# Optimization experiments

Hardware: AMD Instinct MI355X
Metric: run time of the kernel (lower is better)

## Reference

```python
import jax, jax.numpy as jnp
import numpy as np

TABLE_SZ = 2 ** 14
FEAT_DIM = 2
NUM_LEVELS = 16
MIN_RES = 16.0
MAX_RES = 512.0
B = 1 << 20

# corner order v0..v7 from get_nearest_vertices_coords (z-ascending, ccw)
OFFSETS = jnp.array([[0, 0, 0], [1, 0, 0], [1, 1, 0], [0, 1, 0],
                     [0, 0, 1], [1, 0, 1], [1, 1, 1], [0, 1, 1]], dtype=jnp.int32)


def setup_inputs() -> dict:
    key = jax.random.key(0)
    kx, kt = jax.random.split(key)
    x = jax.random.uniform(kx, (B, 3), dtype=jnp.float32)  # coords in [0,1)
    # RandomUniform(-1e-4, 1e-4) initializer for all 16 tables, stacked
    tables = jax.random.uniform(kt, (NUM_LEVELS, TABLE_SZ, FEAT_DIM),
                                dtype=jnp.float32, minval=-1e-4, maxval=1e-4)
    return {"x": x, "tables": tables}


def reference(x, tables):
    # per-level resolutions: floor(min_res * b**l), b geometric growth factor
    b = jnp.exp((jnp.log(MAX_RES) - jnp.log(MIN_RES)) / (NUM_LEVELS - 1))
    res = jnp.floor(MIN_RES * b ** jnp.arange(NUM_LEVELS, dtype=jnp.float32))  # [L]

    # NOTE: original computes interp weights from the UNSCALED position
    # (position - floor(position)); since x in [0,1) this equals x. Faithful.
    w = x - jnp.floor(x)  # [B,3]
    off = OFFSETS.astype(bool)[None]  # [1,8,3]
    # trilinear weight per corner: prod over xyz of (w if offset else 1-w)
    cw = jnp.prod(jnp.where(off, w[:, None, :], 1.0 - w[:, None, :]), axis=-1)  # [B,8]

    P1 = jnp.uint32(2654435761)
    P2 = jnp.uint32(805459861)
    TS = jnp.uint32(TABLE_SZ)

    def level(carry, lvl):
        table, r = lvl  # [T,F], scalar
        sp = r * x  # [B,3]
        low = jnp.floor(sp).astype(jnp.int32)
        high = jnp.ceil(sp).astype(jnp.int32)
        corners = jnp.where(off, high[:, None, :], low[:, None, :]).astype(jnp.uint32)  # [B,8,3]
        # spatial hash: x ^ (p1*y) ^ (p2*z) mod table_sz (uint32 wraparound;
        # table_sz is a power of two so this matches int32-wrap + floormod)
        h = (corners[..., 0] ^ (P1 * corners[..., 1]) ^ (P2 * corners[..., 2])) % TS
        feats = table[h.astype(jnp.int32)]  # gather -> [B,8,F]
        return carry, jnp.einsum('bkf,bk->bf', feats, cw)  # [B,F]

    _, outs = jax.lax.scan(level, None, (tables, res))  # [L,B,F]
    # matches tf.concat over levels along feature axis
    return jnp.transpose(outs, (1, 0, 2)).reshape(x.shape[0], NUM_LEVELS * FEAT_DIM)
```

## Files before the change

kernel.cpp:

```cpp
#include <hip/hip_runtime.h>
#include <cmath>

#define TABLE_SZ 16384
#define NLEV 16
#define BLOCK 256
#define PPT 4
#define HALF 8

struct ResArr { float r[NLEV]; };

__global__ __launch_bounds__(256) void cvt_tables(
    const float* __restrict__ src, uint32_t* __restrict__ dst, int n_entries)
{
    int i = blockIdx.x * blockDim.x + threadIdx.x;
    int e = i * 4;
    if (e + 3 < n_entries) {
        const float4* s4 = (const float4*)(src) + i * 2;
        float4 a = s4[0], b = s4[1];
        uint32_t o[4];
        float v[8] = {a.x,a.y,a.z,a.w,b.x,b.y,b.z,b.w};
        #pragma unroll
        for (int k = 0; k < 4; ++k) {
            uint32_t lo = __float_as_uint(v[2*k+0]);
            uint32_t hi = __float_as_uint(v[2*k+1]);
            lo = (lo + 0x7FFFu + ((lo >> 16) & 1u)) >> 16;
            hi = (hi + 0x7FFFu + ((hi >> 16) & 1u)) & 0xFFFF0000u;
            o[k] = lo | hi;
        }
        *(uint4*)(dst + e) = make_uint4(o[0], o[1], o[2], o[3]);
    }
}

template <typename T>
__device__ __forceinline__ void stage_level(const T* __restrict__ gsrc,
                                            size_t level_bytes, int l,
                                            void* lds, int tid, int wid)
{
    const char* gbase = (const char*)gsrc + (size_t)l * level_bytes;
    const int rounds = (int)(level_bytes / (BLOCK * 16));
    #pragma unroll
    for (int j = 0; j < 16; ++j) {
        if (j >= rounds) break;
        uint32_t goff = (uint32_t)(j * (BLOCK * 16) + tid * 16);
        uint32_t loff = (uint32_t)(j * (BLOCK * 16) + wid * 1024);
        __builtin_amdgcn_global_load_lds(
            (const __attribute__((address_space(1))) uint32_t*)(gbase + goff),
            (__attribute__((address_space(3))) uint32_t*)((char*)lds + loff),
            16, 0, 0);
    }
}

__device__ __forceinline__ float2 level_accum_bf(const uint32_t* tab, float r,
                                                 float px, float py, float pz)
{
    const uint32_t P1 = 2654435761u, P2 = 805459861u;
    const uint32_t m  = TABLE_SZ - 1u;

    float ax = 1.0f - px, ay = 1.0f - py, az = 1.0f - pz;
    float sx = r*px, sy = r*py, sz = r*pz;
    uint32_t lx = (uint32_t)(int32_t)floorf(sx);
    uint32_t hx = (uint32_t)(int32_t)ceilf(sx);
    uint32_t ly = (uint32_t)(int32_t)floorf(sy);
    uint32_t hy = (uint32_t)(int32_t)ceilf(sy);
    uint32_t lz = (uint32_t)(int32_t)floorf(sz);
    uint32_t hz = (uint32_t)(int32_t)ceilf(sz);
    uint32_t yl = P1*ly, yh = P1*hy;
    uint32_t zl = P2*lz, zh = P2*hz;

    float a0, a1;
    {
        uint32_t v0 = tab[(lx ^ yl ^ zl) & m];
        uint32_t v1 = tab[(hx ^ yl ^ zl) & m];
        uint32_t v2 = tab[(hx ^ yh ^ zl) & m];
        uint32_t v3 = tab[(lx ^ yh ^ zl) & m];
        float cw0 = (ax*ay)*az;
        float cw1 = (px*ay)*az;
        float cw2 = (px*py)*az;
        float cw3 = (ax*py)*az;
        a0  = __uint_as_float(v0 << 16)        * cw0;
        a1  = __uint_as_float(v0 & 0xFFFF0000u) * cw0;
        a0 += __uint_as_float(v1 << 16)        * cw1;
        a1 += __uint_as_float(v1 & 0xFFFF0000u) * cw1;
        a0 += __uint_as_float(v2 << 16)        * cw2;
        a1 += __uint_as_float(v2 & 0xFFFF0000u) * cw2;
        a0 += __uint_as_float(v3 << 16)        * cw3;
        a1 += __uint_as_float(v3 & 0xFFFF0000u) * cw3;
    }
    {
        uint32_t v4 = tab[(lx ^ yl ^ zh) & m];
        uint32_t v5 = tab[(hx ^ yl ^ zh) & m];
        uint32_t v6 = tab[(hx ^ yh ^ zh) & m];
        uint32_t v7 = tab[(lx ^ yh ^ zh) & m];
        float cw4 = (ax*ay)*pz;
        float cw5 = (px*ay)*pz;
        float cw6 = (px*py)*pz;
        float cw7 = (ax*py)*pz;
        a0 += __uint_as_float(v4 << 16)        * cw4;
        a1 += __uint_as_float(v4 & 0xFFFF0000u) * cw4;
        a0 += __uint_as_float(v5 << 16)        * cw5;
        a1 += __uint_as_float(v5 & 0xFFFF0000u) * cw5;
        a0 += __uint_as_float(v6 << 16)        * cw6;
        a1 += __uint_as_float(v6 & 0xFFFF0000u) * cw6;
        a0 += __uint_as_float(v7 << 16)        * cw7;
        a1 += __uint_as_float(v7 & 0xFFFF0000u) * cw7;
    }
    return make_float2(a0, a1);
}

__device__ __forceinline__ float2 level_accum_f32(const float2* tab, float r,
                                                  float px, float py, float pz)
{
    const uint32_t P1 = 2654435761u, P2 = 805459861u;
    const uint32_t m  = TABLE_SZ - 1u;
    float ax = 1.0f - px, ay = 1.0f - py, az = 1.0f - pz;
    float sx = r*px, sy = r*py, sz = r*pz;
    uint32_t lx = (uint32_t)(int32_t)floorf(sx);
    uint32_t hx = (uint32_t)(int32_t)ceilf(sx);
    uint32_t ly = (uint32_t)(int32_t)floorf(sy);
    uint32_t hy = (uint32_t)(int32_t)ceilf(sy);
    uint32_t lz = (uint32_t)(int32_t)floorf(sz);
    uint32_t hz = (uint32_t)(int32_t)ceilf(sz);
    uint32_t yl = P1*ly, yh = P1*hy;
    uint32_t zl = P2*lz, zh = P2*hz;
    float a0, a1;
    {
        float2 f0 = tab[(lx ^ yl ^ zl) & m];
        float2 f1 = tab[(hx ^ yl ^ zl) & m];
        float2 f2 = tab[(hx ^ yh ^ zl) & m];
        float2 f3 = tab[(lx ^ yh ^ zl) & m];
        float cw0 = (ax*ay)*az, cw1 = (px*ay)*az, cw2 = (px*py)*az, cw3 = (ax*py)*az;
        a0  = f0.x*cw0;  a1  = f0.y*cw0;
        a0 += f1.x*cw1;  a1 += f1.y*cw1;
        a0 += f2.x*cw2;  a1 += f2.y*cw2;
        a0 += f3.x*cw3;  a1 += f3.y*cw3;
    }
    {
        float2 f4 = tab[(lx ^ yl ^ zh) & m];
        float2 f5 = tab[(hx ^ yl ^ zh) & m];
        float2 f6 = tab[(hx ^ yh ^ zh) & m];
        float2 f7 = tab[(lx ^ yh ^ zh) & m];
        float cw4 = (ax*ay)*pz, cw5 = (px*ay)*pz, cw6 = (px*py)*pz, cw7 = (ax*py)*pz;
        a0 += f4.x*cw4;  a1 += f4.y*cw4;
        a0 += f5.x*cw5;  a1 += f5.y*cw5;
        a0 += f6.x*cw6;  a1 += f6.y*cw6;
        a0 += f7.x*cw7;  a1 += f7.y*cw7;
    }
    return make_float2(a0, a1);
}

__global__ __launch_bounds__(BLOCK) void mrhe_bf(
    const float* __restrict__ x,
    const uint32_t* __restrict__ tb,
    float* __restrict__ out,
    ResArr res, int B)
{
    __shared__ uint32_t tab[TABLE_SZ];

    const int tid  = threadIdx.x;
    const int wid  = tid >> 6;
    const int base = blockIdx.x * (BLOCK * PPT);

    float px[PPT], py[PPT], pz[PPT];
    #pragma unroll
    for (int p = 0; p < PPT; ++p) {
        int idx = base + p * BLOCK + tid;
        size_t j = (idx < B) ? (size_t)idx : 0;
        px[p] = x[3*j+0]; py[p] = x[3*j+1]; pz[p] = x[3*j+2];
    }

    #pragma unroll
    for (int half = 0; half < NLEV / HALF; ++half) {
        float o[PPT][2*HALF];

        #pragma unroll
        for (int hl = 0; hl < HALF; ++hl) {
            const int l = half * HALF + hl;
            __syncthreads();
            stage_level(tb, (size_t)TABLE_SZ * 4, l, tab, tid, wid);
            __syncthreads();

            const float r = res.r[l];
            #pragma unroll
            for (int p = 0; p < PPT; ++p) {
                float2 a = level_accum_bf(tab, r, px[p], py[p], pz[p]);
                o[p][2*hl+0] = a.x;
                o[p][2*hl+1] = a.y;
            }
        }

        #pragma unroll
        for (int p = 0; p < PPT; ++p) {
            int idx = base + p * BLOCK + tid;
            if (idx < B) {
                float* po = out + (size_t)idx * (2*NLEV) + half * (2*HALF);
                #pragma unroll
                for (int j = 0; j < (2*HALF)/4; ++j) {
                    float4 v;
                    v.x = o[p][4*j+0]; v.y = o[p][4*j+1];
                    v.z = o[p][4*j+2]; v.w = o[p][4*j+3];
                    ((float4*)po)[j] = v;
                }
            }
        }
    }
}

#define PPTF 2
__global__ __launch_bounds__(BLOCK) void mrhe_f32(
    const float* __restrict__ x,
    const float* __restrict__ tables,
    float* __restrict__ out,
    ResArr res, int B)
{
    __shared__ float2 tab[TABLE_SZ];

    const int tid  = threadIdx.x;
    const int wid  = tid >> 6;
    const int base = blockIdx.x * (BLOCK * PPTF);

    float px[PPTF], py[PPTF], pz[PPTF];
    #pragma unroll
    for (int p = 0; p < PPTF; ++p) {
        int idx = base + p * BLOCK + tid;
        size_t j = (idx < B) ? (size_t)idx : 0;
        px[p] = x[3*j+0]; py[p] = x[3*j+1]; pz[p] = x[3*j+2];
    }

    #pragma unroll
    for (int half = 0; half < NLEV / HALF; ++half) {
        float o[PPTF][2*HALF];
        #pragma unroll
        for (int hl = 0; hl < HALF; ++hl) {
            const int l = half * HALF + hl;
            __syncthreads();
            {
                const char* gbase = (const char*)tables + (size_t)l * (TABLE_SZ * 8);
                #pragma unroll
                for (int j = 0; j < (TABLE_SZ * 8) / (BLOCK * 16); ++j) {
                    uint32_t goff = (uint32_t)(j * (BLOCK * 16) + tid * 16);
                    uint32_t loff = (uint32_t)(j * (BLOCK * 16) + wid * 1024);
                    __builtin_amdgcn_global_load_lds(
                        (const __attribute__((address_space(1))) uint32_t*)(gbase + goff),
                        (__attribute__((address_space(3))) uint32_t*)((char*)tab + loff),
                        16, 0, 0);
                }
            }
            __syncthreads();
            const float r = res.r[l];
            #pragma unroll
            for (int p = 0; p < PPTF; ++p) {
                float2 a = level_accum_f32(tab, r, px[p], py[p], pz[p]);
                o[p][2*hl+0] = a.x;
                o[p][2*hl+1] = a.y;
            }
        }
        #pragma unroll
        for (int p = 0; p < PPTF; ++p) {
            int idx = base + p * BLOCK + tid;
            if (idx < B) {
                float* po = out + (size_t)idx * (2*NLEV) + half * (2*HALF);
                #pragma unroll
                for (int j = 0; j < (2*HALF)/4; ++j) {
                    float4 v;
                    v.x = o[p][4*j+0]; v.y = o[p][4*j+1];
                    v.z = o[p][4*j+2]; v.w = o[p][4*j+3];
                    ((float4*)po)[j] = v;
                }
            }
        }
    }
}

extern "C" void kernel_launch(void* const* d_in, const int* in_sizes, int n_in,
                              void* d_out, int out_size, void* d_ws, size_t ws_size,
                              hipStream_t stream)
{
    const float* x      = (const float*)d_in[0];
    const float* tables = (const float*)d_in[1];
    float* out = (float*)d_out;
    int B = in_sizes[0] / 3;

    ResArr res;
    float bgrow = expf((logf(512.0f) - logf(16.0f)) / 15.0f);
    for (int l = 0; l < NLEV; ++l)
        res.r[l] = floorf(16.0f * powf(bgrow, (float)l));

    const int n_entries = NLEV * TABLE_SZ;
    const size_t need = (size_t)n_entries * 4;

    if (ws_size >= need && d_ws) {
        uint32_t* tb = (uint32_t*)d_ws;
        hipLaunchKernelGGL(cvt_tables, dim3(n_entries/4/256), dim3(256), 0, stream,
                           tables, tb, n_entries);
        int per_block = BLOCK * PPT;
        int grid = (B + per_block - 1) / per_block;
        hipLaunchKernelGGL(mrhe_bf, dim3(grid), dim3(BLOCK), 0, stream,
                           x, tb, out, res, B);
    } else {
        int per_block = BLOCK * PPTF;
        int grid = (B + per_block - 1) / per_block;
        hipLaunchKernelGGL(mrhe_f32, dim3(grid), dim3(BLOCK), 0, stream,
                           x, tables, out, res, B);
    }
}
```

Before: 133.8 us.

## Double-buffer per-level hash table staging in LDS to overlap loads with gathers

Replaces the single LDS table buffer with two buffers. The next level's table is prefetched with global_load_lds while the current level is interpolated, using manual vmcnt waits and raw s_barrier in place of the two __syncthreads per level. The aim is to hide the table staging latency behind the gather and accumulate work. The cost is that LDS use per block doubles to 128KB, which likely limits the CU to a single 256-thread block and leaves fewer waves to hide LDS gather latency.

```diff
diff --git a/kernel.cpp b/kernel.cpp
--- a/kernel.cpp
+++ b/kernel.cpp
@@ -31,21 +31,17 @@
     }
 }
 
-template <typename T>
-__device__ __forceinline__ void stage_level(const T* __restrict__ gsrc,
-                                            size_t level_bytes, int l,
-                                            void* lds, int tid, int wid)
-{
-    const char* gbase = (const char*)gsrc + (size_t)l * level_bytes;
-    const int rounds = (int)(level_bytes / (BLOCK * 16));
-    #pragma unroll
-    for (int j = 0; j < 16; ++j) {
-        if (j >= rounds) break;
+__device__ __forceinline__ void stage_bf(const uint32_t* __restrict__ tb, int l,
+                                         uint32_t* buf, int tid, int wid)
+{
+    const char* gbase = (const char*)tb + (size_t)l * (TABLE_SZ * 4);
+    #pragma unroll
+    for (int j = 0; j < (TABLE_SZ * 4) / (BLOCK * 16); ++j) {
         uint32_t goff = (uint32_t)(j * (BLOCK * 16) + tid * 16);
         uint32_t loff = (uint32_t)(j * (BLOCK * 16) + wid * 1024);
         __builtin_amdgcn_global_load_lds(
             (const __attribute__((address_space(1))) uint32_t*)(gbase + goff),
-            (__attribute__((address_space(3))) uint32_t*)((char*)lds + loff),
+            (__attribute__((address_space(3))) uint32_t*)((char*)buf + loff),
             16, 0, 0);
     }
 }
@@ -77,13 +73,13 @@
         float cw1 = (px*ay)*az;
         float cw2 = (px*py)*az;
         float cw3 = (ax*py)*az;
-        a0  = __uint_as_float(v0 << 16)        * cw0;
+        a0  = __uint_as_float(v0 << 16)         * cw0;
         a1  = __uint_as_float(v0 & 0xFFFF0000u) * cw0;
-        a0 += __uint_as_float(v1 << 16)        * cw1;
+        a0 += __uint_as_float(v1 << 16)         * cw1;
         a1 += __uint_as_float(v1 & 0xFFFF0000u) * cw1;
-        a0 += __uint_as_float(v2 << 16)        * cw2;
+        a0 += __uint_as_float(v2 << 16)         * cw2;
         a1 += __uint_as_float(v2 & 0xFFFF0000u) * cw2;
-        a0 += __uint_as_float(v3 << 16)        * cw3;
+        a0 += __uint_as_float(v3 << 16)         * cw3;
         a1 += __uint_as_float(v3 & 0xFFFF0000u) * cw3;
     }
     {
@@ -95,13 +91,13 @@
         float cw5 = (px*ay)*pz;
         float cw6 = (px*py)*pz;
         float cw7 = (ax*py)*pz;
-        a0 += __uint_as_float(v4 << 16)        * cw4;
+        a0 += __uint_as_float(v4 << 16)         * cw4;
         a1 += __uint_as_float(v4 & 0xFFFF0000u) * cw4;
-        a0 += __uint_as_float(v5 << 16)        * cw5;
+        a0 += __uint_as_float(v5 << 16)         * cw5;
         a1 += __uint_as_float(v5 & 0xFFFF0000u) * cw5;
-        a0 += __uint_as_float(v6 << 16)        * cw6;
+        a0 += __uint_as_float(v6 << 16)         * cw6;
         a1 += __uint_as_float(v6 & 0xFFFF0000u) * cw6;
-        a0 += __uint_as_float(v7 << 16)        * cw7;
+        a0 += __uint_as_float(v7 << 16)         * cw7;
         a1 += __uint_as_float(v7 & 0xFFFF0000u) * cw7;
     }
     return make_float2(a0, a1);
@@ -148,13 +144,13 @@
     return make_float2(a0, a1);
 }
 
-__global__ __launch_bounds__(BLOCK) void mrhe_bf(
+__global__ __launch_bounds__(BLOCK) void mrhe_bf_db(
     const float* __restrict__ x,
     const uint32_t* __restrict__ tb,
     float* __restrict__ out,
     ResArr res, int B)
 {
-    __shared__ uint32_t tab[TABLE_SZ];
+    __shared__ uint32_t tab[2][TABLE_SZ];
 
     const int tid  = threadIdx.x;
     const int wid  = tid >> 6;
@@ -168,40 +164,48 @@
         px[p] = x[3*j+0]; py[p] = x[3*j+1]; pz[p] = x[3*j+2];
     }
 
-    #pragma unroll
-    for (int half = 0; half < NLEV / HALF; ++half) {
-        float o[PPT][2*HALF];
-
+    stage_bf(tb, 0, tab[0], tid, wid);
+
+    float o[PPT][2*HALF];
+
+    #pragma unroll
+    for (int l = 0; l < NLEV; ++l) {
+        if (l + 1 < NLEV) {
+            stage_bf(tb, l + 1, tab[(l + 1) & 1], tid, wid);
+            asm volatile("s_waitcnt vmcnt(16)" ::: "memory");
+        } else {
+            asm volatile("s_waitcnt vmcnt(0)" ::: "memory");
+        }
+        asm volatile("s_barrier" ::: "memory");
+
+        const float r = res.r[l];
+        const uint32_t* buf = tab[l & 1];
         #pragma unroll
-        for (int hl = 0; hl < HALF; ++hl) {
-            const int l = half * HALF + hl;
-            __syncthreads();
-            stage_level(tb, (size_t)TABLE_SZ * 4, l, tab, tid, wid);
-            __syncthreads();
-
-            const float r = res.r[l];
+        for (int p = 0; p < PPT; ++p) {
+            float2 a = level_accum_bf(buf, r, px[p], py[p], pz[p]);
+            o[p][2*(l & 7) + 0] = a.x;
+            o[p][2*(l & 7) + 1] = a.y;
+        }
+
+        if ((l & 7) == 7) {
+            const int half = l >> 3;
             #pragma unroll
             for (int p = 0; p < PPT; ++p) {
-                float2 a = level_accum_bf(tab, r, px[p], py[p], pz[p]);
-                o[p][2*hl+0] = a.x;
-                o[p][2*hl+1] = a.y;
-            }
-        }
-
-        #pragma unroll
-        for (int p = 0; p < PPT; ++p) {
-            int idx = base + p * BLOCK + tid;
-            if (idx < B) {
-                float* po = out + (size_t)idx * (2*NLEV) + half * (2*HALF);
-                #pragma unroll
-                for (int j = 0; j < (2*HALF)/4; ++j) {
-                    float4 v;
-                    v.x = o[p][4*j+0]; v.y = o[p][4*j+1];
-                    v.z = o[p][4*j+2]; v.w = o[p][4*j+3];
-                    ((float4*)po)[j] = v;
+                int idx = base + p * BLOCK + tid;
+                if (idx < B) {
+                    float* po = out + (size_t)idx * (2*NLEV) + half * (2*HALF);
+                    #pragma unroll
+                    for (int j = 0; j < (2*HALF)/4; ++j) {
+                        float4 v;
+                        v.x = o[p][4*j+0]; v.y = o[p][4*j+1];
+                        v.z = o[p][4*j+2]; v.w = o[p][4*j+3];
+                        ((float4*)po)[j] = v;
+                    }
                 }
             }
         }
+
+        asm volatile("s_barrier" ::: "memory");
     }
 }
 
@@ -294,7 +298,7 @@
                            tables, tb, n_entries);
         int per_block = BLOCK * PPT;
         int grid = (B + per_block - 1) / per_block;
-        hipLaunchKernelGGL(mrhe_bf, dim3(grid), dim3(BLOCK), 0, stream,
+        hipLaunchKernelGGL(mrhe_bf_db, dim3(grid), dim3(BLOCK), 0, stream,
                            x, tb, out, res, B);
     } else {
         int per_block = BLOCK * PPTF;
```

Measured after the change: 116.1 us. 13.2% less time.
